# Optimization experiments

Measured on AMD Instinct MI355X. Metric: run time of the kernel, lower is better.

The kernel has to match this reference:

```python
import jax, jax.numpy as jnp
import numpy as np

N = 262144          # flattened tokens (batch * seq)
D = 256             # bert_hidden_units
C = 50001           # num_items + 1


def setup_inputs() -> dict:
    key = jax.random.key(0)
    k1, k2, k3, k4 = jax.random.split(key, 4)
    inputs_row = jax.random.normal(k1, (N, D), dtype=jnp.float32)
    center = jax.random.normal(k2, (C, D), dtype=jnp.float32)
    target_row = jax.random.randint(k3, (N,), 0, C, dtype=jnp.int64)
    target = jax.random.randint(k4, (4096,), 0, C, dtype=jnp.int64)
    return {"inputs_row": inputs_row, "center": center,
            "target_row": target_row, "target": target}


def reference(inputs_row, center, target_row, target):
    # Fused scatter-mean replacement of the per-class Python loop:
    # for i in unique(target): center[i] = mean(inputs_row[target_row == i])
    num_classes = center.shape[0]
    sums = jax.ops.segment_sum(inputs_row, target_row, num_segments=num_classes)          # [C, D]
    counts = jax.ops.segment_sum(jnp.ones((inputs_row.shape[0],), inputs_row.dtype),
                                 target_row, num_segments=num_classes)                   # [C]
    mean = sums / jnp.where(counts > 0, counts, 1.0)[:, None]                            # [C, D]
    # only classes appearing in `target` are considered, and only those with
    # a nonzero row_mask (counts > 0) actually overwrite center[i]
    present = jnp.zeros((num_classes,), dtype=bool).at[target].set(True)
    upd = present & (counts > 0)
    return jnp.where(upd[:, None], mean, center)
```

## Files before the change

### kernel.cpp

```cpp
#include <hip/hip_runtime.h>

#define N_TOK 262144
#define DDIM  256
#define CCLS  50001
#define SCAN_BLOCK 1024
#define NSCAN_BLOCKS ((CCLS + SCAN_BLOCK - 1) / SCAN_BLOCK)

__global__ void present_kernel(const int* __restrict__ tgt, int n,
                               int* __restrict__ present) {
    int i = blockIdx.x * blockDim.x + threadIdx.x;
    if (i < n) present[tgt[i]] = 1;
}

__global__ void count_kernel(const int* __restrict__ trow,
                             const int* __restrict__ present,
                             int* __restrict__ counts) {
    int i = blockIdx.x * blockDim.x + threadIdx.x;
    if (i < N_TOK) {
        int t = trow[i];
        if (present[t]) atomicAdd(&counts[t], 1);
    }
}

__global__ void scan_blocks(const int* __restrict__ counts,
                            int* __restrict__ offsets,
                            int* __restrict__ block_tot) {
    __shared__ int sm[SCAN_BLOCK];
    int i = blockIdx.x * SCAN_BLOCK + threadIdx.x;
    int v = (i < CCLS) ? counts[i] : 0;
    sm[threadIdx.x] = v;
    __syncthreads();
    int acc = v;
    for (int off = 1; off < SCAN_BLOCK; off <<= 1) {
        int t = (threadIdx.x >= (unsigned)off) ? sm[threadIdx.x - off] : 0;
        __syncthreads();
        acc += t;
        sm[threadIdx.x] = acc;
        __syncthreads();
    }
    if (i < CCLS) offsets[i] = acc - v;
    if (threadIdx.x == SCAN_BLOCK - 1) block_tot[blockIdx.x] = acc;
}

__global__ void scan_totals(int* __restrict__ block_tot) {
    int lane = threadIdx.x;
    int v = block_tot[lane];
    int orig = v;
    for (int off = 1; off < 64; off <<= 1) {
        int t = __shfl_up(v, off);
        if (lane >= off) v += t;
    }
    block_tot[lane] = v - orig;
}

__global__ void add_block_offsets(int* __restrict__ offsets,
                                  const int* __restrict__ block_tot) {
    int i = blockIdx.x * SCAN_BLOCK + threadIdx.x;
    if (i < CCLS) offsets[i] += block_tot[blockIdx.x];
}

__global__ void scatter_kernel(const int* __restrict__ trow,
                               const int* __restrict__ present,
                               int* __restrict__ offsets,
                               int* __restrict__ perm) {
    int i = blockIdx.x * blockDim.x + threadIdx.x;
    if (i < N_TOK) {
        int t = trow[i];
        if (present[t]) {
            int p = atomicAdd(&offsets[t], 1);
            perm[p] = i;
        }
    }
}

__global__ void out_kernel(const float* __restrict__ in,
                           const float* __restrict__ center,
                           const int* __restrict__ counts,
                           const int* __restrict__ present,
                           const int* __restrict__ offsets,
                           const int* __restrict__ perm,
                           float* __restrict__ out) {
    const int wid  = threadIdx.x >> 6;
    const int lane = threadIdx.x & 63;
    const int c = blockIdx.x * 4 + wid;
    if (c >= CCLS) return;

    const int cnt = counts[c];
    const bool upd = (present[c] != 0) && (cnt > 0);
    const long long o4 = (long long)c * (DDIM / 4) + lane;

    float4 r;
    if (upd) {
        const int base = offsets[c] - cnt;
        float4 acc = {0.f, 0.f, 0.f, 0.f};
        for (int k = 0; k < cnt; ++k) {
            const int row = perm[base + k];
            const float4 v =
                reinterpret_cast<const float4*>(in)[(long long)row * (DDIM / 4) + lane];
            acc.x += v.x; acc.y += v.y; acc.z += v.z; acc.w += v.w;
        }
        const float inv = 1.0f / (float)cnt;
        r.x = acc.x * inv; r.y = acc.y * inv; r.z = acc.z * inv; r.w = acc.w * inv;
    } else {
        r = reinterpret_cast<const float4*>(center)[o4];
    }
    reinterpret_cast<float4*>(out)[o4] = r;
}

extern "C" void kernel_launch(void* const* d_in, const int* in_sizes, int n_in,
                              void* d_out, int out_size, void* d_ws, size_t ws_size,
                              hipStream_t stream) {
    const float* inputs_row = (const float*)d_in[0];
    const float* center     = (const float*)d_in[1];
    const int*   target_row = (const int*)d_in[2];
    const int*   target     = (const int*)d_in[3];
    const int    n_target   = in_sizes[3];

    float* out = (float*)d_out;

    int* counts    = (int*)d_ws;
    int* present   = counts + CCLS;
    int* block_tot = present + CCLS;
    int* offsets   = block_tot + 64;
    int* perm      = offsets + CCLS;

    hipMemsetAsync(d_ws, 0, (size_t)(2 * CCLS + 64) * sizeof(int), stream);

    present_kernel<<<(n_target + 255) / 256, 256, 0, stream>>>(target, n_target, present);
    count_kernel<<<(N_TOK + 255) / 256, 256, 0, stream>>>(target_row, present, counts);
    scan_blocks<<<NSCAN_BLOCKS, SCAN_BLOCK, 0, stream>>>(counts, offsets, block_tot);
    scan_totals<<<1, 64, 0, stream>>>(block_tot);
    add_block_offsets<<<NSCAN_BLOCKS, SCAN_BLOCK, 0, stream>>>(offsets, block_tot);
    scatter_kernel<<<(N_TOK + 255) / 256, 256, 0, stream>>>(target_row, present, offsets, perm);

    const int out_blocks = (CCLS + 3) / 4;
    out_kernel<<<out_blocks, 256, 0, stream>>>(inputs_row, center, counts, present,
                                               offsets, perm, out);
}
```

Before: 51.50 us.

## Replace count/scan/scatter bucketing with atomic linked lists per class

Replaces the per-class count, three-kernel prefix scan and scatter pipeline with per-class linked lists built by atomicExch on a head array, with each token storing the previous head in a next array. The present flags are set in the same build kernel, and an init kernel replaces the memset. Cutting from seven launches plus a memset down to three is meant to remove launch overhead and the scan passes. In exchange, lists are built for every token, not only those in present classes, and the output kernel now walks a dependent pointer chain, which serialises the row loads.

```diff
diff --git a/kernel.cpp b/kernel.cpp
--- a/kernel.cpp
+++ b/kernel.cpp
@@ -3,101 +3,53 @@
 #define N_TOK 262144
 #define DDIM  256
 #define CCLS  50001
-#define SCAN_BLOCK 1024
-#define NSCAN_BLOCKS ((CCLS + SCAN_BLOCK - 1) / SCAN_BLOCK)
 
-__global__ void present_kernel(const int* __restrict__ tgt, int n,
-                               int* __restrict__ present) {
+__global__ void init_kernel(int* __restrict__ heads, int* __restrict__ present) {
     int i = blockIdx.x * blockDim.x + threadIdx.x;
-    if (i < n) present[tgt[i]] = 1;
-}
-
-__global__ void count_kernel(const int* __restrict__ trow,
-                             const int* __restrict__ present,
-                             int* __restrict__ counts) {
-    int i = blockIdx.x * blockDim.x + threadIdx.x;
-    if (i < N_TOK) {
-        int t = trow[i];
-        if (present[t]) atomicAdd(&counts[t], 1);
+    if (i < CCLS) {
+        heads[i] = -1;
+        present[i] = 0;
     }
 }
 
-__global__ void scan_blocks(const int* __restrict__ counts,
-                            int* __restrict__ offsets,
-                            int* __restrict__ block_tot) {
-    __shared__ int sm[SCAN_BLOCK];
-    int i = blockIdx.x * SCAN_BLOCK + threadIdx.x;
-    int v = (i < CCLS) ? counts[i] : 0;
-    sm[threadIdx.x] = v;
-    __syncthreads();
-    int acc = v;
-    for (int off = 1; off < SCAN_BLOCK; off <<= 1) {
-        int t = (threadIdx.x >= (unsigned)off) ? sm[threadIdx.x - off] : 0;
-        __syncthreads();
-        acc += t;
-        sm[threadIdx.x] = acc;
-        __syncthreads();
-    }
-    if (i < CCLS) offsets[i] = acc - v;
-    if (threadIdx.x == SCAN_BLOCK - 1) block_tot[blockIdx.x] = acc;
-}
-
-__global__ void scan_totals(int* __restrict__ block_tot) {
-    int lane = threadIdx.x;
-    int v = block_tot[lane];
-    int orig = v;
-    for (int off = 1; off < 64; off <<= 1) {
-        int t = __shfl_up(v, off);
-        if (lane >= off) v += t;
-    }
-    block_tot[lane] = v - orig;
-}
-
-__global__ void add_block_offsets(int* __restrict__ offsets,
-                                  const int* __restrict__ block_tot) {
-    int i = blockIdx.x * SCAN_BLOCK + threadIdx.x;
-    if (i < CCLS) offsets[i] += block_tot[blockIdx.x];
-}
-
-__global__ void scatter_kernel(const int* __restrict__ trow,
-                               const int* __restrict__ present,
-                               int* __restrict__ offsets,
-                               int* __restrict__ perm) {
+__global__ void build_kernel(const int* __restrict__ trow,
+                             const int* __restrict__ tgt, int n_tgt,
+                             int* __restrict__ heads,
+                             int* __restrict__ next,
+                             int* __restrict__ present) {
     int i = blockIdx.x * blockDim.x + threadIdx.x;
     if (i < N_TOK) {
-        int t = trow[i];
-        if (present[t]) {
-            int p = atomicAdd(&offsets[t], 1);
-            perm[p] = i;
-        }
+        const int t = trow[i];
+        const int old = atomicExch(&heads[t], i);
+        next[i] = old;
     }
+    if (i < n_tgt) present[tgt[i]] = 1;
 }
 
 __global__ void out_kernel(const float* __restrict__ in,
                            const float* __restrict__ center,
-                           const int* __restrict__ counts,
+                           const int* __restrict__ heads,
+                           const int* __restrict__ next,
                            const int* __restrict__ present,
-                           const int* __restrict__ offsets,
-                           const int* __restrict__ perm,
                            float* __restrict__ out) {
     const int wid  = threadIdx.x >> 6;
     const int lane = threadIdx.x & 63;
     const int c = blockIdx.x * 4 + wid;
     if (c >= CCLS) return;
 
-    const int cnt = counts[c];
-    const bool upd = (present[c] != 0) && (cnt > 0);
+    const int head = heads[c];
+    const bool upd = (present[c] != 0) && (head != -1);
     const long long o4 = (long long)c * (DDIM / 4) + lane;
 
     float4 r;
     if (upd) {
-        const int base = offsets[c] - cnt;
         float4 acc = {0.f, 0.f, 0.f, 0.f};
-        for (int k = 0; k < cnt; ++k) {
-            const int row = perm[base + k];
+        int cnt = 0;
+        for (int row = head; row != -1; row = next[row]) {
             const float4 v =
                 reinterpret_cast<const float4*>(in)[(long long)row * (DDIM / 4) + lane];
             acc.x += v.x; acc.y += v.y; acc.z += v.z; acc.w += v.w;
+            ++cnt;
         }
         const float inv = 1.0f / (float)cnt;
         r.x = acc.x * inv; r.y = acc.y * inv; r.z = acc.z * inv; r.w = acc.w * inv;
@@ -118,22 +70,13 @@
 
     float* out = (float*)d_out;
 
-    int* counts    = (int*)d_ws;
-    int* present   = counts + CCLS;
-    int* block_tot = present + CCLS;
-    int* offsets   = block_tot + 64;
-    int* perm      = offsets + CCLS;
+    int* heads   = (int*)d_ws;
+    int* present = heads + CCLS;
+    int* next    = present + CCLS;
 
-    hipMemsetAsync(d_ws, 0, (size_t)(2 * CCLS + 64) * sizeof(int), stream);
-
-    present_kernel<<<(n_target + 255) / 256, 256, 0, stream>>>(target, n_target, present);
-    count_kernel<<<(N_TOK + 255) / 256, 256, 0, stream>>>(target_row, present, counts);
-    scan_blocks<<<NSCAN_BLOCKS, SCAN_BLOCK, 0, stream>>>(counts, offsets, block_tot);
-    scan_totals<<<1, 64, 0, stream>>>(block_tot);
-    add_block_offsets<<<NSCAN_BLOCKS, SCAN_BLOCK, 0, stream>>>(offsets, block_tot);
-    scatter_kernel<<<(N_TOK + 255) / 256, 256, 0, stream>>>(target_row, present, offsets, perm);
-
-    const int out_blocks = (CCLS + 3) / 4;
-    out_kernel<<<out_blocks, 256, 0, stream>>>(inputs_row, center, counts, present,
-                                               offsets, perm, out);
+    init_kernel<<<(CCLS + 255) / 256, 256, 0, stream>>>(heads, present);
+    build_kernel<<<(N_TOK + 255) / 256, 256, 0, stream>>>(target_row, target, n_target,
+                                                          heads, next, present);
+    out_kernel<<<(CCLS + 3) / 4, 256, 0, stream>>>(inputs_row, center, heads, next,
+                                                   present, out);
 }
```

New measurement: 44.76 us. 13.1% less time.
